# Performance work log

Measured on AMD Instinct MI355X. Metric: run time of the kernel, lower is better.

## Reference

```python
import jax, jax.numpy as jnp
import numpy as np

D_MODEL = 1024
NUM_HEADS = 16
HEAD_DIM = D_MODEL // NUM_HEADS
SCALE = 1.0 / (HEAD_DIM ** 0.5)


def setup_inputs() -> dict:
    key = jax.random.key(0)
    ks = jax.random.split(key, 5)
    std = 1.0 / np.sqrt(D_MODEL)
    x = jax.random.normal(ks[0], (2, 2048, D_MODEL), dtype=jnp.float32)
    Wq = jax.random.normal(ks[1], (D_MODEL, D_MODEL), dtype=jnp.float32) * std
    Wk = jax.random.normal(ks[2], (D_MODEL, D_MODEL), dtype=jnp.float32) * std
    Wv = jax.random.normal(ks[3], (D_MODEL, D_MODEL), dtype=jnp.float32) * std
    Wo = jax.random.normal(ks[4], (D_MODEL, D_MODEL), dtype=jnp.float32) * std
    zeros = jnp.zeros((D_MODEL,), dtype=jnp.float32)
    return {"x": x, "Wq": Wq, "bq": zeros, "Wk": Wk, "bk": zeros,
            "Wv": Wv, "bv": zeros, "Wo": Wo, "bo": zeros}


def reference(x, Wq, bq, Wk, bk, Wv, bv, Wo, bo):
    B, S, D = x.shape
    H, hd = NUM_HEADS, HEAD_DIM
    # Linear projections (torch Linear: y = x @ W.T + b)
    q = (x @ Wq.T + bq).reshape(B, S, H, hd).transpose(0, 2, 1, 3)  # [B,H,S,hd]
    k = (x @ Wk.T + bk).reshape(B, S, H, hd).transpose(0, 2, 1, 3)
    v = (x @ Wv.T + bv).reshape(B, S, H, hd).transpose(0, 2, 1, 3)
    scores = jnp.einsum('bhqd,bhkd->bhqk', q, k) * SCALE  # [B,H,S,S]
    causal = jnp.tril(jnp.ones((S, S), dtype=bool))
    scores = jnp.where(causal, scores, -jnp.inf)
    attn = jax.nn.softmax(scores, axis=-1)
    out = jnp.einsum('bhqk,bhkd->bhqd', attn, v)  # [B,H,S,hd]
    out = out.transpose(0, 2, 1, 3).reshape(B, S, D)
    return out @ Wo.T + bo
```

## Files before the change

### kernel.cpp

```cpp
#include <hip/hip_runtime.h>
#include <hip/hip_bf16.h>


typedef __attribute__((ext_vector_type(8))) short short8;
typedef __attribute__((ext_vector_type(4))) float f32x4;
typedef __attribute__((ext_vector_type(8))) unsigned short u16x8;
typedef __attribute__((ext_vector_type(4))) unsigned short u16x4;

#define QSCALE 0.1803368801111244f
#define MFMA16(a, b, c) __builtin_amdgcn_mfma_f32_16x16x32_bf16(a, b, c, 0, 0, 0)

__device__ __forceinline__ unsigned short f2bf(float f) {
  unsigned int u = __float_as_uint(f);
  u += 0x7fffu + ((u >> 16) & 1u);
  return (unsigned short)(u >> 16);
}

__device__ __forceinline__ void gload_lds16(const void* g, void* l) {
  __builtin_amdgcn_global_load_lds(
      (const __attribute__((address_space(1))) unsigned int*)g,
      (__attribute__((address_space(3))) unsigned int*)l, 16, 0, 0);
}

__global__ __launch_bounds__(256) void convert_all_kernel(
    const float* __restrict__ x, const float* __restrict__ wq,
    const float* __restrict__ wk, const float* __restrict__ wv,
    const float* __restrict__ wo, unsigned short* __restrict__ xb,
    unsigned short* __restrict__ wqkv, unsigned short* __restrict__ wob) {
  const int b = blockIdx.x, tid = threadIdx.x;
  const float* src;
  unsigned short* dst;
  int i;
  if (b < 4096) { src = x; dst = xb; i = b * 256 + tid; }
  else {
    const int r = b - 4096, seg = r >> 10;
    i = (r & 1023) * 256 + tid;
    src = seg == 0 ? wq : (seg == 1 ? wk : (seg == 2 ? wv : wo));
    dst = seg == 3 ? wob : wqkv + (size_t)seg * 1048576;
  }
  float4 v = ((const float4*)src)[i];
  u16x4 o = {f2bf(v.x), f2bf(v.y), f2bf(v.z), f2bf(v.w)};
  *(u16x4*)(dst + (size_t)i * 4) = o;
}

template<int NF>
__device__ __forceinline__ void gemm_db_mainloop(
    const unsigned short* __restrict__ A, const unsigned short* __restrict__ B,
    int tm, int tn, unsigned short* As0, unsigned short* Bs0,
    f32x4 (&acc)[4][NF]) {
  constexpr int BN = NF * 32;
  const int tid = threadIdx.x;
  const int w = tid >> 6, l = tid & 63;
  const int wr = (w >> 1) * 64, wc = (w & 1) * (BN / 2);
  const int srow = l >> 2;
  const int schunk = (l & 3) * 8;
  const int rl = l & 15, kl = (l >> 4) * 8;
  const int K = 1024;
  unsigned short* As1 = As0 + 128 * 32;
  unsigned short* Bs1 = Bs0 + BN * 32;

#define STAGE_TILE(AP, BP, KOFF)                                               \
  {                                                                            \
    _Pragma("unroll") for (int c = 0; c < 2; ++c) {                            \
      const int rowb = w * 32 + c * 16;                                        \
      gload_lds16(A + (size_t)(tm + rowb + srow) * K + (KOFF) + schunk,        \
                  (AP) + rowb * 32);                                           \
    }                                                                          \
    _Pragma("unroll") for (int c = 0; c < BN / 64; ++c) {                      \
      const int rowb = w * (BN / 4) + c * 16;                                  \
      gload_lds16(B + (size_t)(tn + rowb + srow) * K + (KOFF) + schunk,        \
                  (BP) + rowb * 32);                                           \
    }                                                                          \
  }

  STAGE_TILE(As0, Bs0, 0)
  __syncthreads();
  int p = 0;
  for (int k0 = 0; k0 < K; k0 += 32) {
    unsigned short* Ac = p ? As1 : As0;
    unsigned short* Bc = p ? Bs1 : Bs0;
    if (k0 + 32 < K) {
      unsigned short* An = p ? As0 : As1;
      unsigned short* Bn = p ? Bs0 : Bs1;
      STAGE_TILE(An, Bn, k0 + 32)
    }
    short8 af[4], bf[NF];
#pragma unroll
    for (int m = 0; m < 4; ++m) af[m] = *(const short8*)&Ac[(wr + m * 16 + rl) * 32 + kl];
#pragma unroll
    for (int n = 0; n < NF; ++n) bf[n] = *(const short8*)&Bc[(wc + n * 16 + rl) * 32 + kl];
#pragma unroll
    for (int m = 0; m < 4; ++m)
#pragma unroll
      for (int n = 0; n < NF; ++n)
        acc[m][n] = MFMA16(af[m], bf[n], acc[m][n]);
    __syncthreads();
    p ^= 1;
  }
#undef STAGE_TILE
}

__global__ __launch_bounds__(256) void gemm_qkv_kernel(
    const unsigned short* __restrict__ xb, const unsigned short* __restrict__ wqkv,
    const float* __restrict__ bq, const float* __restrict__ bk, const float* __restrict__ bv,
    unsigned short* __restrict__ Qb, unsigned short* __restrict__ Kb,
    unsigned short* __restrict__ VTb) {
  __shared__ unsigned short As[2 * 128 * 32], Bs[2 * 128 * 32];
  f32x4 acc[4][4] = {};
  const int flat = blockIdx.x;
  const int xcd = flat & 7, loc = flat >> 3;
  const int bn = xcd * 3 + loc % 3, bm = loc / 3;
  const int tm = bm * 128, tn = bn * 128;
  gemm_db_mainloop<4>(xb, wqkv, tm, tn, As, Bs, acc);

  const int tid = threadIdx.x, w = tid >> 6, l = tid & 63;
  const int wr = (w >> 1) * 64, wc = (w & 1) * 64;
  const int rl = l & 15, hi = l >> 4;
  const int proj = tn >> 10;
  const float* bias = proj == 0 ? bq : (proj == 1 ? bk : bv);
#pragma unroll
  for (int m = 0; m < 4; ++m) {
    const int row0 = tm + wr + m * 16 + hi * 4;
    const int b2 = row0 >> 11, s2 = row0 & 2047;
#pragma unroll
    for (int n = 0; n < 4; ++n) {
      const int col = (tn & 1023) + wc + n * 16 + rl;
      const int h = col >> 6, d = col & 63;
      const float bi = bias[col];
      if (proj == 2) {
        u16x4 pv = {f2bf(acc[m][n][0] + bi), f2bf(acc[m][n][1] + bi),
                    f2bf(acc[m][n][2] + bi), f2bf(acc[m][n][3] + bi)};
        *(u16x4*)&VTb[((size_t)((b2 * 16 + h) * 64 + d)) * 2048 + s2] = pv;
      } else {
        const float sc = (proj == 0) ? QSCALE : 1.0f;
        unsigned short* dst = (proj == 0) ? Qb : Kb;
#pragma unroll
        for (int i = 0; i < 4; ++i)
          dst[((size_t)(b2 * 16 + h) * 2048 + (s2 + i)) * 64 + d] =
              f2bf((acc[m][n][i] + bi) * sc);
      }
    }
  }
}

template<bool DIAG>
__device__ __forceinline__ void softmax_pack(
    const f32x4 s[4], float& l_i, char* ps,
    int rl, int hi, int swz, int qrow, int kv0) {
  float p[4][4];
  float rs = 0.f;
#pragma unroll
  for (int f = 0; f < 4; ++f)
#pragma unroll
    for (int i = 0; i < 4; ++i) {
      float sv = s[f][i];
      if (DIAG) sv = (kv0 + f * 16 + hi * 4 + i <= qrow) ? sv : -1e30f;
      const float e = __builtin_amdgcn_exp2f(sv);
      p[f][i] = e;
      rs += e;
    }
  rs += __shfl_xor(rs, 16, 64);
  rs += __shfl_xor(rs, 32, 64);
  l_i += rs;
#pragma unroll
  for (int f = 0; f < 4; ++f) {
    u16x4 pv = {f2bf(p[f][0]), f2bf(p[f][1]), f2bf(p[f][2]), f2bf(p[f][3])};
    *(u16x4*)(ps + rl * 128 + ((f * 32 + hi * 8) ^ swz)) = pv;
  }
}

template<bool L_ON, bool L_DIAG, bool H_DIAG>
__device__ __forceinline__ void attn_stage(
    const char* kb, const char* vb, char* psH, char* psL,
    const short8 qfH[2], const short8 qfL[2],
    f32x4 oH[4], f32x4 oL[4], float& lH, float& lL,
    int rl, int hi, int swz, int qrH, int qrL, int kv0, int w) {
  const int fvH = H_DIAG ? (w + 1) : 4;
  f32x4 sH[4] = {}, sL[4] = {};
  __builtin_amdgcn_s_setprio(1);
#pragma unroll
  for (int f = 0; f < 4; ++f) {
    if (H_DIAG && f >= fvH) continue;
    const char* rowp = kb + (f * 16 + rl) * 128;
#pragma unroll
    for (int kc = 0; kc < 2; ++kc) {
      short8 kf = *(const short8*)(rowp + ((kc * 64 + hi * 16) ^ swz));
      sH[f] = MFMA16(kf, qfH[kc], sH[f]);
      if (L_ON && (!L_DIAG || f < w + 1)) sL[f] = MFMA16(kf, qfL[kc], sL[f]);
    }
  }
  __builtin_amdgcn_s_setprio(0);
  softmax_pack<H_DIAG>(sH, lH, psH, rl, hi, swz, qrH, kv0);
  if (L_ON) softmax_pack<L_DIAG>(sL, lL, psL, rl, hi, swz, qrL, kv0);

  const int kcvH = H_DIAG ? ((w >= 2) ? 2 : 1) : 2;
  const int kcvL = (L_ON && L_DIAG) ? ((w >= 2) ? 2 : 1) : 2;
  __builtin_amdgcn_s_setprio(1);
#pragma unroll
  for (int kc = 0; kc < 2; ++kc) {
    if (H_DIAG && kc >= kcvH) continue;
    short8 paH = *(const short8*)(psH + rl * 128 + ((kc * 64 + hi * 16) ^ swz));
    const bool lpv = L_ON && kc < kcvL;
    short8 paL = {};
    if (lpv) paL = *(const short8*)(psL + rl * 128 + ((kc * 64 + hi * 16) ^ swz));
#pragma unroll
    for (int fd = 0; fd < 4; ++fd) {
      short8 vf = *(const short8*)(vb + (fd * 16 + rl) * 128 + ((kc * 64 + hi * 16) ^ swz));
      oH[fd] = MFMA16(vf, paH, oH[fd]);
      if (lpv) oL[fd] = MFMA16(vf, paL, oL[fd]);
    }
  }
  __builtin_amdgcn_s_setprio(0);
}

__global__ __launch_bounds__(256) void flash_kernel(
    const unsigned short* __restrict__ Q, const unsigned short* __restrict__ K,
    const unsigned short* __restrict__ VT, unsigned short* __restrict__ AO) {
  __shared__ unsigned short KbS[2][64 * 64];
  __shared__ unsigned short VbS[2][64 * 64];
  __shared__ unsigned short PsS[4][2][16 * 64];

  const int tid = threadIdx.x;
  const int w = tid >> 6, l = tid & 63;
  const int rl = l & 15, hi = l >> 4;
  const int swz = (rl & 7) << 4;
  const int bid = blockIdx.x;
  const int g = bid & 7, r = bid >> 3;
  const int bh = g * 4 + (r & 3);
  const int pr = r >> 2;
  const int qtH = 31 - pr, qtL = pr;
  const size_t head_off = (size_t)bh * 2048 * 64;

  const int qrH = qtH * 64 + w * 16 + rl;
  const int qrL = qtL * 64 + w * 16 + rl;

  short8 qfH[2], qfL[2];
  {
    const unsigned short* qp = Q + head_off + (size_t)qrH * 64 + hi * 8;
    qfH[0] = *(const short8*)qp;
    qfH[1] = *(const short8*)(qp + 32);
    qp = Q + head_off + (size_t)qrL * 64 + hi * 8;
    qfL[0] = *(const short8*)qp;
    qfL[1] = *(const short8*)(qp + 32);
  }

  f32x4 oH[4] = {}, oL[4] = {};
  float lH = 0.f, lL = 0.f;

  const int sr = tid >> 2;
  const int swzW = (sr & 7) << 4;
  const int cb0 = (tid & 3) * 32;
  const int kwoff0 = sr * 128 + (cb0 ^ swzW);
  const int kwoff1 = sr * 128 + ((cb0 + 16) ^ swzW);
  const unsigned short* kbase = K + head_off + (size_t)sr * 64 + (tid & 3) * 16;
  const unsigned short* vbase = VT + ((size_t)(bh * 64 + sr)) * 2048 + (tid & 3) * 16;

  u16x8 kra = *(const u16x8*)kbase;
  u16x8 krb = *(const u16x8*)(kbase + 8);
  u16x8 vra = *(const u16x8*)vbase;
  u16x8 vrb = *(const u16x8*)(vbase + 8);
  {
    char* kd = (char*)KbS;
    char* vd = (char*)VbS;
    *(u16x8*)(kd + kwoff0) = kra;
    *(u16x8*)(kd + kwoff1) = krb;
    *(u16x8*)(vd + kwoff0) = vra;
    *(u16x8*)(vd + kwoff1) = vrb;
  }
  kra = *(const u16x8*)(kbase + 4096);
  krb = *(const u16x8*)(kbase + 4096 + 8);
  vra = *(const u16x8*)(vbase + 64);
  vrb = *(const u16x8*)(vbase + 64 + 8);
  __syncthreads();

  char* psH = (char*)&PsS[w][0][0];
  char* psL = (char*)&PsS[w][1][0];

  for (int t = 0; t <= qtH; ++t) {
    const int cur = t & 1;
    const char* kb = (const char*)KbS + cur * 8192;
    const char* vb = (const char*)VbS + cur * 8192;
    const int kv0 = t * 64;

    if (t < qtL)
      attn_stage<true, false, false>(kb, vb, psH, psL, qfH, qfL, oH, oL, lH, lL,
                                     rl, hi, swz, qrH, qrL, kv0, w);
    else if (t == qtL)
      attn_stage<true, true, false>(kb, vb, psH, psL, qfH, qfL, oH, oL, lH, lL,
                                    rl, hi, swz, qrH, qrL, kv0, w);
    else if (t < qtH)
      attn_stage<false, false, false>(kb, vb, psH, psL, qfH, qfL, oH, oL, lH, lL,
                                      rl, hi, swz, qrH, qrL, kv0, w);
    else
      attn_stage<false, false, true>(kb, vb, psH, psL, qfH, qfL, oH, oL, lH, lL,
                                     rl, hi, swz, qrH, qrL, kv0, w);

    if (t < qtH) {
      char* kd = (char*)KbS + (cur ^ 1) * 8192;
      char* vd = (char*)VbS + (cur ^ 1) * 8192;
      *(u16x8*)(kd + kwoff0) = kra;
      *(u16x8*)(kd + kwoff1) = krb;
      *(u16x8*)(vd + kwoff0) = vra;
      *(u16x8*)(vd + kwoff1) = vrb;
      if (t + 2 <= qtH) {
        const size_t ko = (size_t)(t + 2) * 4096;
        kra = *(const u16x8*)(kbase + ko);
        krb = *(const u16x8*)(kbase + ko + 8);
        vra = *(const u16x8*)(vbase + (t + 2) * 64);
        vrb = *(const u16x8*)(vbase + (t + 2) * 64 + 8);
      }
    }
    __syncthreads();
  }

  const float invH = 1.f / lH, invL = 1.f / lL;
  const size_t orowH = (size_t)(bh >> 4) * 2048 + qrH;
  const size_t orowL = (size_t)(bh >> 4) * 2048 + qrL;
  const int hcol = (bh & 15) * 64;
#pragma unroll
  for (int fd = 0; fd < 4; ++fd) {
    u16x4 a = {f2bf(oH[fd][0] * invH), f2bf(oH[fd][1] * invH),
               f2bf(oH[fd][2] * invH), f2bf(oH[fd][3] * invH)};
    *(u16x4*)&AO[orowH * 1024 + hcol + fd * 16 + hi * 4] = a;
    u16x4 b = {f2bf(oL[fd][0] * invL), f2bf(oL[fd][1] * invL),
               f2bf(oL[fd][2] * invL), f2bf(oL[fd][3] * invL)};
    *(u16x4*)&AO[orowL * 1024 + hcol + fd * 16 + hi * 4] = b;
  }
}

__global__ __launch_bounds__(256) void gemm_out_kernel(
    const unsigned short* __restrict__ AOb, const unsigned short* __restrict__ wob,
    const float* __restrict__ bo, float* __restrict__ out) {
  __shared__ unsigned short As[2 * 128 * 32], Bs[2 * 64 * 32];
  f32x4 acc[4][2] = {};
  const int flat = blockIdx.x;
  const int xcd = flat & 7, loc = flat >> 3;
  const int bn = xcd * 2 + (loc & 1), bm = loc >> 1;
  const int tm = bm * 128, tn = bn * 64;
  gemm_db_mainloop<2>(AOb, wob, tm, tn, As, Bs, acc);
  const int tid = threadIdx.x, w = tid >> 6, l = tid & 63;
  const int wr = (w >> 1) * 64, wc = (w & 1) * 32;
  const int rl = l & 15, hi = l >> 4;
#pragma unroll
  for (int m = 0; m < 4; ++m) {
    const int row0 = tm + wr + m * 16 + hi * 4;
#pragma unroll
    for (int n = 0; n < 2; ++n) {
      const int col = tn + wc + n * 16 + rl;
      const float bo_ = bo[col];
#pragma unroll
      for (int i = 0; i < 4; ++i)
        out[(size_t)(row0 + i) * 1024 + col] = acc[m][n][i] + bo_;
    }
  }
}

extern "C" void kernel_launch(void* const* d_in, const int* in_sizes, int n_in,
                              void* d_out, int out_size, void* d_ws, size_t ws_size,
                              hipStream_t stream) {
  const float* x  = (const float*)d_in[0];
  const float* Wq = (const float*)d_in[1];
  const float* bq = (const float*)d_in[2];
  const float* Wk = (const float*)d_in[3];
  const float* bk = (const float*)d_in[4];
  const float* Wv = (const float*)d_in[5];
  const float* bv = (const float*)d_in[6];
  const float* Wo = (const float*)d_in[7];
  const float* bo = (const float*)d_in[8];
  float* out = (float*)d_out;

  unsigned short* ws = (unsigned short*)d_ws;
  unsigned short* XB   = ws;
  unsigned short* WQKV = ws + 4194304;
  unsigned short* WOB  = ws + 7340032;
  unsigned short* QB   = ws + 8388608;
  unsigned short* KB   = ws + 12582912;
  unsigned short* VTB  = ws + 16777216;
  unsigned short* AOB  = XB;

  convert_all_kernel<<<8192, 256, 0, stream>>>(x, Wq, Wk, Wv, Wo, XB, WQKV, WOB);
  gemm_qkv_kernel<<<768, 256, 0, stream>>>(XB, WQKV, bq, bk, bv, QB, KB, VTB);
  flash_kernel<<<512, 256, 0, stream>>>(QB, KB, VTB, AOB);
  gemm_out_kernel<<<512, 256, 0, stream>>>(AOB, WOB, bo, out);
}
```

Measured before the change: 197.8 us.

## Rewrite QKV GEMM with 256x256 tiles, 512 threads and triple-buffered LDS

```diff
diff --git a/kernel.cpp b/kernel.cpp
--- a/kernel.cpp
+++ b/kernel.cpp
@@ -43,6 +43,100 @@
   *(u16x4*)(dst + (size_t)i * 4) = o;
 }
 
+__global__ __launch_bounds__(512, 2) void gemm_qkv_kernel(
+    const unsigned short* __restrict__ xb, const unsigned short* __restrict__ wqkv,
+    const float* __restrict__ bq, const float* __restrict__ bk, const float* __restrict__ bv,
+    unsigned short* __restrict__ Qb, unsigned short* __restrict__ Kb,
+    unsigned short* __restrict__ VTb) {
+  __shared__ unsigned short As[3 * 256 * 32];
+  __shared__ unsigned short Bs[3 * 256 * 32];
+
+  const int tid = threadIdx.x;
+  const int w = tid >> 6, l = tid & 63;
+  const int wm = w >> 2, wn = w & 3;
+  const int rl = l & 15, hi = l >> 4;
+
+  const int wg = (blockIdx.x & 7) * 24 + (blockIdx.x >> 3);
+  const int bm = wg / 12, bn = wg % 12;
+  const int tm = bm * 256, tn = bn * 256;
+
+  const unsigned short* Ag = xb + (size_t)(tm + (tid >> 2)) * 1024 + (tid & 3) * 8;
+  const unsigned short* Bg = wqkv + (size_t)(tn + (tid >> 2)) * 1024 + (tid & 3) * 8;
+  const int wst = w * 512;
+
+#define QKV_STAGE(slot, k0)                                                    \
+  {                                                                            \
+    gload_lds16(Ag + (k0), As + (slot) * 8192 + wst);                          \
+    gload_lds16(Ag + 128 * 1024 + (k0), As + (slot) * 8192 + 4096 + wst);      \
+    gload_lds16(Bg + (k0), Bs + (slot) * 8192 + wst);                          \
+    gload_lds16(Bg + 128 * 1024 + (k0), Bs + (slot) * 8192 + 4096 + wst);      \
+  }
+
+  f32x4 acc[8][4] = {};
+
+  QKV_STAGE(0, 0)
+  QKV_STAGE(1, 32)
+  asm volatile("s_waitcnt vmcnt(4)" ::: "memory");
+  __builtin_amdgcn_s_barrier();
+  asm volatile("" ::: "memory");
+
+  const int abase = (wm * 128 + rl) * 32 + hi * 8;
+  const int bbase = (wn * 64 + rl) * 32 + hi * 8;
+
+  int sl = 0, sn = 2;
+  for (int t = 0; t < 32; ++t) {
+    if (t < 30) QKV_STAGE(sn, (t + 2) * 32)
+
+    const unsigned short* Ap = As + sl * 8192;
+    const unsigned short* Bp = Bs + sl * 8192;
+    short8 bfr[4];
+#pragma unroll
+    for (int n = 0; n < 4; ++n) bfr[n] = *(const short8*)&Bp[bbase + n * 512];
+    short8 afr[8];
+#pragma unroll
+    for (int m = 0; m < 8; ++m) afr[m] = *(const short8*)&Ap[abase + m * 512];
+#pragma unroll
+    for (int m = 0; m < 8; ++m)
+#pragma unroll
+      for (int n = 0; n < 4; ++n)
+        acc[m][n] = MFMA16(afr[m], bfr[n], acc[m][n]);
+
+    if (t < 30) asm volatile("s_waitcnt vmcnt(4)" ::: "memory");
+    else        asm volatile("s_waitcnt vmcnt(0)" ::: "memory");
+    __builtin_amdgcn_s_barrier();
+    asm volatile("" ::: "memory");
+    sl = (sl == 2) ? 0 : sl + 1;
+    sn = (sn == 2) ? 0 : sn + 1;
+  }
+#undef QKV_STAGE
+
+  const int proj = tn >> 10;
+  const float* bias = proj == 0 ? bq : (proj == 1 ? bk : bv);
+#pragma unroll
+  for (int m = 0; m < 8; ++m) {
+    const int row0 = tm + wm * 128 + m * 16 + hi * 4;
+    const int b2 = row0 >> 11, s2 = row0 & 2047;
+#pragma unroll
+    for (int n = 0; n < 4; ++n) {
+      const int col = (tn & 1023) + wn * 64 + n * 16 + rl;
+      const int h = col >> 6, d = col & 63;
+      const float bi = bias[col];
+      if (proj == 2) {
+        u16x4 pv = {f2bf(acc[m][n][0] + bi), f2bf(acc[m][n][1] + bi),
+                    f2bf(acc[m][n][2] + bi), f2bf(acc[m][n][3] + bi)};
+        *(u16x4*)&VTb[((size_t)((b2 * 16 + h) * 64 + d)) * 2048 + s2] = pv;
+      } else {
+        const float sc = (proj == 0) ? QSCALE : 1.0f;
+        unsigned short* dst = (proj == 0) ? Qb : Kb;
+#pragma unroll
+        for (int i = 0; i < 4; ++i)
+          dst[((size_t)(b2 * 16 + h) * 2048 + (s2 + i)) * 64 + d] =
+              f2bf((acc[m][n][i] + bi) * sc);
+      }
+    }
+  }
+}
+
 template<int NF>
 __device__ __forceinline__ void gemm_db_mainloop(
     const unsigned short* __restrict__ A, const unsigned short* __restrict__ B,
@@ -100,49 +194,6 @@
 #undef STAGE_TILE
 }
 
-__global__ __launch_bounds__(256) void gemm_qkv_kernel(
-    const unsigned short* __restrict__ xb, const unsigned short* __restrict__ wqkv,
-    const float* __restrict__ bq, const float* __restrict__ bk, const float* __restrict__ bv,
-    unsigned short* __restrict__ Qb, unsigned short* __restrict__ Kb,
-    unsigned short* __restrict__ VTb) {
-  __shared__ unsigned short As[2 * 128 * 32], Bs[2 * 128 * 32];
-  f32x4 acc[4][4] = {};
-  const int flat = blockIdx.x;
-  const int xcd = flat & 7, loc = flat >> 3;
-  const int bn = xcd * 3 + loc % 3, bm = loc / 3;
-  const int tm = bm * 128, tn = bn * 128;
-  gemm_db_mainloop<4>(xb, wqkv, tm, tn, As, Bs, acc);
-
-  const int tid = threadIdx.x, w = tid >> 6, l = tid & 63;
-  const int wr = (w >> 1) * 64, wc = (w & 1) * 64;
-  const int rl = l & 15, hi = l >> 4;
-  const int proj = tn >> 10;
-  const float* bias = proj == 0 ? bq : (proj == 1 ? bk : bv);
-#pragma unroll
-  for (int m = 0; m < 4; ++m) {
-    const int row0 = tm + wr + m * 16 + hi * 4;
-    const int b2 = row0 >> 11, s2 = row0 & 2047;
-#pragma unroll
-    for (int n = 0; n < 4; ++n) {
-      const int col = (tn & 1023) + wc + n * 16 + rl;
-      const int h = col >> 6, d = col & 63;
-      const float bi = bias[col];
-      if (proj == 2) {
-        u16x4 pv = {f2bf(acc[m][n][0] + bi), f2bf(acc[m][n][1] + bi),
-                    f2bf(acc[m][n][2] + bi), f2bf(acc[m][n][3] + bi)};
-        *(u16x4*)&VTb[((size_t)((b2 * 16 + h) * 64 + d)) * 2048 + s2] = pv;
-      } else {
-        const float sc = (proj == 0) ? QSCALE : 1.0f;
-        unsigned short* dst = (proj == 0) ? Qb : Kb;
-#pragma unroll
-        for (int i = 0; i < 4; ++i)
-          dst[((size_t)(b2 * 16 + h) * 2048 + (s2 + i)) * 64 + d] =
-              f2bf((acc[m][n][i] + bi) * sc);
-      }
-    }
-  }
-}
-
 template<bool DIAG>
 __device__ __forceinline__ void softmax_pack(
     const f32x4 s[4], float& l_i, char* ps,
@@ -379,7 +430,7 @@
   unsigned short* AOB  = XB;
 
   convert_all_kernel<<<8192, 256, 0, stream>>>(x, Wq, Wk, Wv, Wo, XB, WQKV, WOB);
-  gemm_qkv_kernel<<<768, 256, 0, stream>>>(XB, WQKV, bq, bk, bv, QB, KB, VTB);
+  gemm_qkv_kernel<<<192, 512, 0, stream>>>(XB, WQKV, bq, bk, bv, QB, KB, VTB);
   flash_kernel<<<512, 256, 0, stream>>>(QB, KB, VTB, AOB);
   gemm_out_kernel<<<512, 256, 0, stream>>>(AOB, WOB, bo, out);
 }
```

Measured after the change: 197.4 us. No clear change (-0.2%).
